# Performance work log

Hardware: AMD Instinct MI355X
Metric: run time of the kernel (lower is better)

The kernel has to match this reference:

```python
import jax, jax.numpy as jnp
import numpy as np

DIM = 1024
B, N = 8, 4096
EPS = 1e-6


def setup_inputs() -> dict:
    key = jax.random.key(0)
    k1, k2, k3, k4 = jax.random.split(key, 4)
    x = jax.random.normal(k1, (B, N, DIM), dtype=jnp.float32)
    # torch nn.Linear weights: W_qkv [3*dim, dim], W_out [dim, dim], b_out [dim]
    s = 1.0 / np.sqrt(DIM)
    W_qkv = jax.random.uniform(k2, (3 * DIM, DIM), jnp.float32, -s, s)
    W_out = jax.random.uniform(k3, (DIM, DIM), jnp.float32, -s, s)
    b_out = jax.random.uniform(k4, (DIM,), jnp.float32, -s, s)
    return {"x": x, "W_qkv": W_qkv, "W_out": W_out, "b_out": b_out}


def reference(x, W_qkv, W_out, b_out):
    # qkv projection (Linear without bias): x @ W_qkv.T -> [B,N,3D]
    qkv = jnp.einsum('bnd,ed->bne', x, W_qkv)
    q, k, v = jnp.split(qkv, 3, axis=-1)
    q = jax.nn.relu(q) + EPS
    k = jax.nn.relu(k) + EPS
    # kv accumulation: [B,D,D]
    kv = jnp.einsum('bnd,bne->bde', k, v)
    # normalizer z: [B,N]
    z = 1.0 / (jnp.einsum('bnd,bd->bn', q, k.sum(axis=1)) + EPS)
    # attn output: [B,N,D]
    attn = jnp.einsum('bnd,bde,bn->bne', q, kv, z)
    # output projection with bias
    return jnp.einsum('bne,fe->bnf', attn, W_out) + b_out
```

## Files before the change

### kernel.cpp

```cpp
#include <hip/hip_runtime.h>


#define EPS 1e-6f

using u16 = unsigned short;
typedef __attribute__((ext_vector_type(4))) float f32x4;
typedef __attribute__((ext_vector_type(8))) __bf16 bf16x8;

__device__ __forceinline__ u16 f2b(float f) {
  unsigned u = __builtin_bit_cast(unsigned, f);
  u += 0x7FFFu + ((u >> 16) & 1u);
  return (u16)(u >> 16);
}
__device__ __forceinline__ float b2f(u16 h) {
  return __builtin_bit_cast(float, (unsigned)h << 16);
}

typedef const __attribute__((address_space(1))) void* gas1_t;
typedef __attribute__((address_space(3))) void* las3_t;

__device__ __forceinline__ void load16_to_lds(const void* g, void* l) {
  __builtin_amdgcn_global_load_lds((gas1_t)g, (las3_t)l, 16, 0, 0);
}

#define BARRIER() do { asm volatile("" ::: "memory"); __builtin_amdgcn_s_barrier(); asm volatile("" ::: "memory"); } while (0)
#define WAITL0()  asm volatile("s_waitcnt lgkmcnt(0)" ::: "memory")
#define WAITV(n)  asm volatile("s_waitcnt vmcnt(" #n ")" ::: "memory")
#define MFMA16(a, b, c) __builtin_amdgcn_mfma_f32_16x16x32_bf16((a), (b), (c), 0, 0, 0)

__device__ __forceinline__ void stage_half(const u16* g, int ld, u16* l,
                                           int r0, int csw, int woff) {
  load16_to_lds(g + (long long)r0 * ld + csw, l + woff);
  load16_to_lds(g + (long long)(r0 + 64) * ld + csw, l + 4096 + woff);
}

template<int MODE>
__global__ __launch_bounds__(512, 2) void gemm256(
    const u16* __restrict__ A, const u16* __restrict__ B, void* __restrict__ Cv,
    int M, int N, int K, int lda, int ldb, int ldc,
    long long sA, long long sB, long long sC,
    const float* __restrict__ zvec, const float* __restrict__ bias,
    u16* __restrict__ kT, u16* __restrict__ vT, float* __restrict__ ksum)
{
  __shared__ __align__(16) u16 shA[32768];
  __shared__ __align__(16) u16 shB[32768];

  const int tid  = threadIdx.x;
  const int lane = tid & 63, wave = tid >> 6;
  const int wr = wave >> 2, wc = wave & 3;
  const int quad = lane >> 4, lc = lane & 15;

  const int TN = gridDim.y;
  const int lin = blockIdx.x + gridDim.x * blockIdx.y;
  const int xcd = lin & 7, g = lin >> 3;
  const int bm = (g / TN) * 8 + xcd;
  const int bn = g % TN;
  const int bz = blockIdx.z;
  const u16* Ab = A + (long long)bz * sA;
  const u16* Bb = B + (long long)bz * sB;

  const int r0   = tid >> 3;
  const int csw  = (((tid & 7) ^ ((tid >> 3) & 7)) << 3);
  const int woff = wave * 512;

  const int ch0 = ((quad ^ (lane & 7)) << 3);
  const int ch1 = (((4 + quad) ^ (lane & 7)) << 3);
  const int aRow = wr * 128 + lc;
  const int bRow = wc * 64 + lc;

  const int NT = K >> 6;

  f32x4 acc[8][4];
  #pragma unroll
  for (int i = 0; i < 8; ++i)
    #pragma unroll
    for (int j = 0; j < 4; ++j) acc[i][j] = f32x4{0.f, 0.f, 0.f, 0.f};

  auto stA = [&](int h, int t) {
    stage_half(Ab + ((long long)bm * 256 + h * 128) * lda + t * 64, lda,
               shA + (t & 1) * 16384 + h * 8192, r0, csw, woff);
  };
  auto stB = [&](int h, int t) {
    stage_half(Bb + ((long long)bn * 256 + h * 128) * ldb + t * 64, ldb,
               shB + (t & 1) * 16384 + h * 8192, r0, csw, woff);
  };

  stA(0, 0); stA(1, 0); stB(0, 0); stB(1, 0);
  if (NT > 1) { stA(0, 1); stA(1, 1); stB(0, 1); WAITV(6); }
  else        { WAITV(0); }
  BARRIER();

  for (int t = 0; t < NT; ++t) {
    const u16* aB = shA + (t & 1) * 16384;
    const u16* bB = shB + (t & 1) * 16384;
    bf16x8 aF[4][2], b01[2][2], b23[2][2];

    #pragma unroll
    for (int i = 0; i < 4; ++i) {
      aF[i][0] = *(const bf16x8*)&aB[(aRow + i * 16) * 64 + ch0];
      aF[i][1] = *(const bf16x8*)&aB[(aRow + i * 16) * 64 + ch1];
    }
    #pragma unroll
    for (int j = 0; j < 2; ++j) {
      b01[j][0] = *(const bf16x8*)&bB[(bRow + j * 16) * 64 + ch0];
      b01[j][1] = *(const bf16x8*)&bB[(bRow + j * 16) * 64 + ch1];
    }
    if (t + 1 < NT) stB(1, t + 1);
    BARRIER(); WAITL0();
    __builtin_amdgcn_s_setprio(1);
    #pragma unroll
    for (int i = 0; i < 4; ++i)
      #pragma unroll
      for (int j = 0; j < 2; ++j) {
        acc[i][j] = MFMA16(aF[i][0], b01[j][0], acc[i][j]);
        acc[i][j] = MFMA16(aF[i][1], b01[j][1], acc[i][j]);
      }
    __builtin_amdgcn_s_setprio(0);
    BARRIER();

    #pragma unroll
    for (int j = 0; j < 2; ++j) {
      b23[j][0] = *(const bf16x8*)&bB[(bRow + (2 + j) * 16) * 64 + ch0];
      b23[j][1] = *(const bf16x8*)&bB[(bRow + (2 + j) * 16) * 64 + ch1];
    }
    BARRIER(); WAITL0();
    __builtin_amdgcn_s_setprio(1);
    #pragma unroll
    for (int i = 0; i < 4; ++i)
      #pragma unroll
      for (int j = 0; j < 2; ++j) {
        acc[i][2 + j] = MFMA16(aF[i][0], b23[j][0], acc[i][2 + j]);
        acc[i][2 + j] = MFMA16(aF[i][1], b23[j][1], acc[i][2 + j]);
      }
    __builtin_amdgcn_s_setprio(0);
    BARRIER();

    #pragma unroll
    for (int i = 0; i < 4; ++i) {
      aF[i][0] = *(const bf16x8*)&aB[(aRow + (4 + i) * 16) * 64 + ch0];
      aF[i][1] = *(const bf16x8*)&aB[(aRow + (4 + i) * 16) * 64 + ch1];
    }
    if (t + 2 < NT) stB(0, t + 2);
    BARRIER(); WAITL0();
    __builtin_amdgcn_s_setprio(1);
    #pragma unroll
    for (int i = 0; i < 4; ++i)
      #pragma unroll
      for (int j = 0; j < 2; ++j) {
        acc[4 + i][j] = MFMA16(aF[i][0], b01[j][0], acc[4 + i][j]);
        acc[4 + i][j] = MFMA16(aF[i][1], b01[j][1], acc[4 + i][j]);
      }
    __builtin_amdgcn_s_setprio(0);
    BARRIER();

    if (t + 2 < NT) { stA(0, t + 2); stA(1, t + 2); }
    BARRIER(); WAITL0();
    __builtin_amdgcn_s_setprio(1);
    #pragma unroll
    for (int i = 0; i < 4; ++i)
      #pragma unroll
      for (int j = 0; j < 2; ++j) {
        acc[4 + i][2 + j] = MFMA16(aF[i][0], b23[j][0], acc[4 + i][2 + j]);
        acc[4 + i][2 + j] = MFMA16(aF[i][1], b23[j][1], acc[4 + i][2 + j]);
      }
    __builtin_amdgcn_s_setprio(0);
    if (t + 2 < NT) { WAITV(6); } else { WAITV(0); }
    BARRIER();
  }

  const long long rowb = (long long)bm * 256 + wr * 128 + quad * 4;
  const int colb = bn * 256 + wc * 64 + lc;

  if (MODE == 0) {
    const int region = colb >> 10;
    if (region == 0) {
      u16* q = (u16*)Cv;
      #pragma unroll
      for (int i = 0; i < 8; ++i)
        #pragma unroll
        for (int j = 0; j < 4; ++j) {
          const int col = colb + j * 16;
          #pragma unroll
          for (int r = 0; r < 4; ++r) {
            const long long row = rowb + i * 16 + r;
            q[row * ldc + col] = f2b(fmaxf(acc[i][j][r], 0.f) + EPS);
          }
        }
    } else {
      const bool isk = (region == 1);
      const int b = (int)(rowb >> 12);
      u16* dst = (isk ? kT : vT) + (long long)b * 1024 * 4096;
      const int nloc = (int)(rowb & 4095);
      #pragma unroll
      for (int j = 0; j < 4; ++j) {
        const int d = colb + j * 16 - region * 1024;
        float s = 0.f;
        #pragma unroll
        for (int i = 0; i < 8; ++i) {
          ushort4 pk;
          #pragma unroll
          for (int r = 0; r < 4; ++r) {
            float v = acc[i][j][r];
            if (isk) { v = fmaxf(v, 0.f) + EPS; s += v; }
            (&pk.x)[r] = f2b(v);
          }
          *(ushort4*)(dst + (long long)d * 4096 + nloc + i * 16) = pk;
        }
        if (isk) {
          s += __shfl_xor(s, 16);
          s += __shfl_xor(s, 32);
          if (quad == 0) atomicAdd(&ksum[b * 1024 + d], s);
        }
      }
    }
  } else if (MODE == 2) {
    float* out = (float*)Cv + (long long)bz * sC;
    #pragma unroll
    for (int i = 0; i < 8; ++i)
      #pragma unroll
      for (int j = 0; j < 4; ++j) {
        const int col = colb + j * 16;
        const float bj = bias[col];
        #pragma unroll
        for (int r = 0; r < 4; ++r) {
          const long long row = rowb + i * 16 + r;
          out[row * ldc + col] = acc[i][j][r] * zvec[(long long)bz * M + row] + bj;
        }
      }
  } else {
    u16* out = (u16*)Cv + (long long)bz * sC;
    #pragma unroll
    for (int i = 0; i < 8; ++i)
      #pragma unroll
      for (int j = 0; j < 4; ++j) {
        const int col = colb + j * 16;
        #pragma unroll
        for (int r = 0; r < 4; ++r) {
          const long long row = rowb + i * 16 + r;
          out[row * ldc + col] = f2b(acc[i][j][r]);
        }
      }
  }
}

template<int MODE>
__global__ __launch_bounds__(256) void gemm_abT(
    const u16* __restrict__ A, const u16* __restrict__ B, void* __restrict__ Cv,
    int M, int N, int K, int lda, int ldb, int ldc,
    long long sA, long long sB, long long sC,
    const float* __restrict__ zvec, const float* __restrict__ bias,
    u16* __restrict__ kT, u16* __restrict__ vT, float* __restrict__ ksum)
{
  __shared__ u16 lA[128 * 32];
  __shared__ u16 lB[128 * 32];
  const int tid  = threadIdx.x;
  const int wave = tid >> 6, lane = tid & 63;
  const int TN = gridDim.y;
  const int lin = blockIdx.x + gridDim.x * blockIdx.y;
  const int xcd = lin & 7, g = lin >> 3;
  const int bm = (g / TN) * 8 + xcd;
  const int bn = g % TN;
  const int bz = blockIdx.z;
  const u16* Ab = A + (long long)bz * sA;
  const u16* Bb = B + (long long)bz * sB;

  const int c0 = wave * 64 + lane;
  const int c1 = 256 + c0;
  const u16* gA0 = Ab + (long long)(bm * 128 + (c0 >> 2)) * lda + (c0 & 3) * 8;
  const u16* gA1 = Ab + (long long)(bm * 128 + (c1 >> 2)) * lda + (c1 & 3) * 8;
  const u16* gB0 = Bb + (long long)(bn * 128 + (c0 >> 2)) * ldb + (c0 & 3) * 8;
  const u16* gB1 = Bb + (long long)(bn * 128 + (c1 >> 2)) * ldb + (c1 & 3) * 8;
  u16* lA0 = &lA[(wave * 64) * 8];
  u16* lA1 = &lA[(256 + wave * 64) * 8];
  u16* lB0 = &lB[(wave * 64) * 8];
  u16* lB1 = &lB[(256 + wave * 64) * 8];

  const int wm = (wave & 1) * 64, wn = (wave >> 1) * 64;
  const int aoff = (wm + (lane & 15)) * 32 + (lane >> 4) * 8;
  const int boff = (wn + (lane & 15)) * 32 + (lane >> 4) * 8;

  f32x4 acc[4][4];
  #pragma unroll
  for (int i = 0; i < 4; i++)
    #pragma unroll
    for (int j = 0; j < 4; j++) acc[i][j] = f32x4{0.f, 0.f, 0.f, 0.f};

  for (int k0 = 0; k0 < K; k0 += 32) {
    load16_to_lds(gA0 + k0, lA0);
    load16_to_lds(gA1 + k0, lA1);
    load16_to_lds(gB0 + k0, lB0);
    load16_to_lds(gB1 + k0, lB1);
    __syncthreads();
    bf16x8 af[4], bfv[4];
    #pragma unroll
    for (int i = 0; i < 4; i++) af[i]  = *(const bf16x8*)&lA[aoff + i * 16 * 32];
    #pragma unroll
    for (int j = 0; j < 4; j++) bfv[j] = *(const bf16x8*)&lB[boff + j * 16 * 32];
    #pragma unroll
    for (int i = 0; i < 4; i++)
      #pragma unroll
      for (int j = 0; j < 4; j++)
        acc[i][j] = MFMA16(af[i], bfv[j], acc[i][j]);
    __syncthreads();
  }

  const int quad = lane >> 4, lc = lane & 15;
  const int rowb = bm * 128 + wm + quad * 4;
  const int colb = bn * 128 + wn + lc;

  #pragma unroll
  for (int i = 0; i < 4; i++) {
    #pragma unroll
    for (int j = 0; j < 4; j++) {
      const int col = colb + j * 16;
      float bj = 0.f;
      if (MODE == 2) bj = bias[col];
      #pragma unroll
      for (int r = 0; r < 4; r++) {
        const int row = rowb + i * 16 + r;
        float v = acc[i][j][r];
        if (MODE == 1) {
          ((u16*)Cv + (long long)bz * sC)[(long long)row * ldc + col] = f2b(v);
        } else if (MODE == 2) {
          float zz = zvec[(long long)bz * M + row];
          ((float*)Cv + (long long)bz * sC)[(long long)row * ldc + col] = v * zz + bj;
        }
      }
    }
  }
  (void)kT; (void)vT; (void)ksum;
}

__global__ void cvt_f32_bf16(const float* __restrict__ s, u16* __restrict__ d, int n4) {
  int i = blockIdx.x * blockDim.x + threadIdx.x;
  int st = gridDim.x * blockDim.x;
  for (; i < n4; i += st) {
    float4 f = ((const float4*)s)[i];
    uint2 o;
    o.x = (unsigned)f2b(f.x) | ((unsigned)f2b(f.y) << 16);
    o.y = (unsigned)f2b(f.z) | ((unsigned)f2b(f.w) << 16);
    ((uint2*)d)[i] = o;
  }
}

__global__ void zero_f32(float* __restrict__ p, int n) {
  int i = blockIdx.x * blockDim.x + threadIdx.x;
  if (i < n) p[i] = 0.f;
}

__global__ void z_kernel(const u16* __restrict__ qbuf, const float* __restrict__ ksum,
                         float* __restrict__ z) {
  const int row  = blockIdx.x * 4 + (threadIdx.x >> 6);
  const int lane = threadIdx.x & 63;
  const int b = row >> 12;
  const uint4* q = (const uint4*)(qbuf + (long long)row * 1024);
  const float* ks = ksum + b * 1024;
  float s = 0.f;
  #pragma unroll
  for (int c = 0; c < 2; c++) {
    int idx = lane + c * 64;
    uint4 d = q[idx];
    unsigned w[4] = {d.x, d.y, d.z, d.w};
    const float* kk = ks + idx * 8;
    #pragma unroll
    for (int qq = 0; qq < 4; qq++)
      s += b2f((u16)(w[qq] & 0xFFFF)) * kk[qq * 2]
         + b2f((u16)(w[qq] >> 16))    * kk[qq * 2 + 1];
  }
  #pragma unroll
  for (int o = 32; o > 0; o >>= 1) s += __shfl_down(s, o);
  if (lane == 0) z[row] = 1.0f / (s + EPS);
}

extern "C" void kernel_launch(void* const* d_in, const int* in_sizes, int n_in,
                              void* d_out, int out_size, void* d_ws, size_t ws_size,
                              hipStream_t stream) {
  const float* x    = (const float*)d_in[0];
  const float* Wqkv = (const float*)d_in[1];
  const float* Wout = (const float*)d_in[2];
  const float* bout = (const float*)d_in[3];

  char* ws = (char*)d_ws;
  u16* x_bf    = (u16*)(ws + 0);
  u16* qbuf    = (u16*)(ws + 67108864);
  u16* kT      = (u16*)(ws + 134217728);
  u16* vT      = (u16*)(ws + 201326592);
  u16* wqkv_bf = (u16*)(ws + 268435456);
  u16* wout_bf = (u16*)(ws + 274726912);
  u16* kv      = (u16*)(ws + 276824064);
  u16* kvwT    = (u16*)(ws + 293601280);
  float* ksum  = (float*)(ws + 310378496);
  float* z     = (float*)(ws + 310411264);

  cvt_f32_bf16<<<4096, 256, 0, stream>>>(x,    x_bf,    33554432 / 4);
  cvt_f32_bf16<<<1024, 256, 0, stream>>>(Wqkv, wqkv_bf,  3145728 / 4);
  cvt_f32_bf16<<<512,  256, 0, stream>>>(Wout, wout_bf,  1048576 / 4);
  zero_f32<<<32, 256, 0, stream>>>(ksum, 8192);

  gemm256<0><<<dim3(128, 12, 1), 512, 0, stream>>>(
      x_bf, wqkv_bf, qbuf, 32768, 3072, 1024, 1024, 1024, 1024,
      0, 0, 0, nullptr, nullptr, kT, vT, ksum);

  z_kernel<<<8192, 256, 0, stream>>>(qbuf, ksum, z);

  gemm_abT<1><<<dim3(8, 8, 8), 256, 0, stream>>>(
      kT, vT, kv, 1024, 1024, 4096, 4096, 4096, 1024,
      4194304, 4194304, 1048576, nullptr, nullptr, nullptr, nullptr, nullptr);

  gemm_abT<1><<<dim3(8, 8, 8), 256, 0, stream>>>(
      wout_bf, kv, kvwT, 1024, 1024, 1024, 1024, 1024, 1024,
      0, 1048576, 1048576, nullptr, nullptr, nullptr, nullptr, nullptr);

  gemm256<2><<<dim3(16, 4, 8), 512, 0, stream>>>(
      qbuf, kvwT, d_out, 4096, 1024, 1024, 1024, 1024, 1024,
      4194304, 1048576, 4194304, z, bout, nullptr, nullptr, nullptr);
}
```

Baseline: 708.6 us.

## Prefetch next tile's A fragments during last MFMA phase of GEMM loop

Moves the LDS read of the first half of A fragments for the next K-tile into the final phase of the current iteration, using a separate register set for the second half so the two can overlap. The global-load wait moves earlier so the next buffer is ready before that prefetch, and a sched_barrier is added after LDS waits to pin the instruction order. The aim is to hide LDS latency at the start of each iteration, at the cost of extra registers that may pressure occupancy at 2 waves per SIMD.

```diff
diff --git a/kernel.cpp b/kernel.cpp
--- a/kernel.cpp
+++ b/kernel.cpp
@@ -24,7 +24,7 @@
 }
 
 #define BARRIER() do { asm volatile("" ::: "memory"); __builtin_amdgcn_s_barrier(); asm volatile("" ::: "memory"); } while (0)
-#define WAITL0()  asm volatile("s_waitcnt lgkmcnt(0)" ::: "memory")
+#define WAITL0()  do { asm volatile("s_waitcnt lgkmcnt(0)" ::: "memory"); __builtin_amdgcn_sched_barrier(0); } while (0)
 #define WAITV(n)  asm volatile("s_waitcnt vmcnt(" #n ")" ::: "memory")
 #define MFMA16(a, b, c) __builtin_amdgcn_mfma_f32_16x16x32_bf16((a), (b), (c), 0, 0, 0)
 
@@ -85,21 +85,23 @@
                shB + (t & 1) * 16384 + h * 8192, r0, csw, woff);
   };
 
+  bf16x8 aF[4][2], aG[4][2], b01[2][2], b23[2][2];
+
   stA(0, 0); stA(1, 0); stB(0, 0); stB(1, 0);
-  if (NT > 1) { stA(0, 1); stA(1, 1); stB(0, 1); WAITV(6); }
+  if (NT > 1) { stB(0, 1); stA(0, 1); stA(1, 1); WAITV(6); }
   else        { WAITV(0); }
   BARRIER();
+  #pragma unroll
+  for (int i = 0; i < 4; ++i) {
+    aF[i][0] = *(const bf16x8*)&shA[(aRow + i * 16) * 64 + ch0];
+    aF[i][1] = *(const bf16x8*)&shA[(aRow + i * 16) * 64 + ch1];
+  }
 
   for (int t = 0; t < NT; ++t) {
     const u16* aB = shA + (t & 1) * 16384;
     const u16* bB = shB + (t & 1) * 16384;
-    bf16x8 aF[4][2], b01[2][2], b23[2][2];
-
-    #pragma unroll
-    for (int i = 0; i < 4; ++i) {
-      aF[i][0] = *(const bf16x8*)&aB[(aRow + i * 16) * 64 + ch0];
-      aF[i][1] = *(const bf16x8*)&aB[(aRow + i * 16) * 64 + ch1];
-    }
+    const u16* aN = shA + ((t + 1) & 1) * 16384;
+
     #pragma unroll
     for (int j = 0; j < 2; ++j) {
       b01[j][0] = *(const bf16x8*)&bB[(bRow + j * 16) * 64 + ch0];
@@ -137,8 +139,8 @@
 
     #pragma unroll
     for (int i = 0; i < 4; ++i) {
-      aF[i][0] = *(const bf16x8*)&aB[(aRow + (4 + i) * 16) * 64 + ch0];
-      aF[i][1] = *(const bf16x8*)&aB[(aRow + (4 + i) * 16) * 64 + ch1];
+      aG[i][0] = *(const bf16x8*)&aB[(aRow + (4 + i) * 16) * 64 + ch0];
+      aG[i][1] = *(const bf16x8*)&aB[(aRow + (4 + i) * 16) * 64 + ch1];
     }
     if (t + 2 < NT) stB(0, t + 2);
     BARRIER(); WAITL0();
@@ -147,24 +149,31 @@
     for (int i = 0; i < 4; ++i)
       #pragma unroll
       for (int j = 0; j < 2; ++j) {
-        acc[4 + i][j] = MFMA16(aF[i][0], b01[j][0], acc[4 + i][j]);
-        acc[4 + i][j] = MFMA16(aF[i][1], b01[j][1], acc[4 + i][j]);
+        acc[4 + i][j] = MFMA16(aG[i][0], b01[j][0], acc[4 + i][j]);
+        acc[4 + i][j] = MFMA16(aG[i][1], b01[j][1], acc[4 + i][j]);
       }
     __builtin_amdgcn_s_setprio(0);
+    if (t + 2 < NT) { WAITV(2); } else { WAITV(0); }
     BARRIER();
 
+    if (t + 1 < NT) {
+      #pragma unroll
+      for (int i = 0; i < 4; ++i) {
+        aF[i][0] = *(const bf16x8*)&aN[(aRow + i * 16) * 64 + ch0];
+        aF[i][1] = *(const bf16x8*)&aN[(aRow + i * 16) * 64 + ch1];
+      }
+    }
     if (t + 2 < NT) { stA(0, t + 2); stA(1, t + 2); }
-    BARRIER(); WAITL0();
+    BARRIER();
     __builtin_amdgcn_s_setprio(1);
     #pragma unroll
     for (int i = 0; i < 4; ++i)
       #pragma unroll
       for (int j = 0; j < 2; ++j) {
-        acc[4 + i][2 + j] = MFMA16(aF[i][0], b23[j][0], acc[4 + i][2 + j]);
-        acc[4 + i][2 + j] = MFMA16(aF[i][1], b23[j][1], acc[4 + i][2 + j]);
+        acc[4 + i][2 + j] = MFMA16(aG[i][0], b23[j][0], acc[4 + i][2 + j]);
+        acc[4 + i][2 + j] = MFMA16(aG[i][1], b23[j][1], acc[4 + i][2 + j]);
       }
     __builtin_amdgcn_s_setprio(0);
-    if (t + 2 < NT) { WAITV(6); } else { WAITV(0); }
     BARRIER();
   }
 
```

Result: no change. 711.5 us (+0.4%).

## Split-K the per-batch KV GEMM with 256-tile kernel and separate reduction

Applied to the files above, without the earlier changes.

Replaces the gemm_abT KV accumulation (K=4096) with the larger 256-tile gemm256 kernel in a new mode that splits K into two halves across 16 z-slices. Each half writes fp32 partials into the now-unused x_bf workspace. A new reduce_kv kernel sums the halves and converts them to bf16. The aim is better per-block efficiency and enough blocks to fill the device, at the cost of an extra kernel launch and a round trip of fp32 partials through memory. Grid remapping also skips the XCD swizzle when gridDim.x < 8.

```diff
diff --git a/kernel.cpp b/kernel.cpp
--- a/kernel.cpp
+++ b/kernel.cpp
@@ -52,12 +52,26 @@
 
   const int TN = gridDim.y;
   const int lin = blockIdx.x + gridDim.x * blockIdx.y;
-  const int xcd = lin & 7, g = lin >> 3;
-  const int bm = (g / TN) * 8 + xcd;
-  const int bn = g % TN;
+  int bm, bn;
+  if (gridDim.x >= 8) {
+    const int xcd = lin & 7, g = lin >> 3;
+    bm = (g / TN) * 8 + xcd;
+    bn = g % TN;
+  } else {
+    bm = blockIdx.x;
+    bn = blockIdx.y;
+  }
   const int bz = blockIdx.z;
-  const u16* Ab = A + (long long)bz * sA;
-  const u16* Bb = B + (long long)bz * sB;
+  const u16* Ab;
+  const u16* Bb;
+  if (MODE == 3) {
+    const int bb = bz & 7, kh = bz >> 3;
+    Ab = A + (long long)bb * sA + kh * 2048;
+    Bb = B + (long long)bb * sB + kh * 2048;
+  } else {
+    Ab = A + (long long)bz * sA;
+    Bb = B + (long long)bz * sB;
+  }
 
   const int r0   = tid >> 3;
   const int csw  = (((tid & 7) ^ ((tid >> 3) & 7)) << 3);
@@ -225,6 +239,19 @@
         for (int r = 0; r < 4; ++r) {
           const long long row = rowb + i * 16 + r;
           out[row * ldc + col] = acc[i][j][r] * zvec[(long long)bz * M + row] + bj;
+        }
+      }
+  } else if (MODE == 3) {
+    float* out = (float*)Cv + (long long)bz * sC;
+    #pragma unroll
+    for (int i = 0; i < 8; ++i)
+      #pragma unroll
+      for (int j = 0; j < 4; ++j) {
+        const int col = colb + j * 16;
+        #pragma unroll
+        for (int r = 0; r < 4; ++r) {
+          const long long row = rowb + i * 16 + r;
+          out[row * ldc + col] = acc[i][j][r];
         }
       }
   } else {
@@ -348,6 +375,23 @@
   if (i < n) p[i] = 0.f;
 }
 
+__global__ void reduce_kv(const float* __restrict__ p, u16* __restrict__ kv) {
+  long long idx = blockIdx.x * blockDim.x + threadIdx.x;
+  const long long st = (long long)gridDim.x * blockDim.x;
+  for (; idx < 2097152; idx += st) {
+    const long long b = idx >> 18;
+    const long long i = idx & 262143;
+    float4 x = ((const float4*)p)[b * 262144 + i];
+    float4 y = ((const float4*)p)[(8 + b) * 262144 + i];
+    float4 s;
+    s.x = x.x + y.x; s.y = x.y + y.y; s.z = x.z + y.z; s.w = x.w + y.w;
+    uint2 o;
+    o.x = (unsigned)f2b(s.x) | ((unsigned)f2b(s.y) << 16);
+    o.y = (unsigned)f2b(s.z) | ((unsigned)f2b(s.w) << 16);
+    ((uint2*)kv)[b * 262144 + i] = o;
+  }
+}
+
 __global__ void z_kernel(const u16* __restrict__ qbuf, const float* __restrict__ ksum,
                          float* __restrict__ z) {
   const int row  = blockIdx.x * 4 + (threadIdx.x >> 6);
@@ -403,9 +447,11 @@
 
   z_kernel<<<8192, 256, 0, stream>>>(qbuf, ksum, z);
 
-  gemm_abT<1><<<dim3(8, 8, 8), 256, 0, stream>>>(
-      kT, vT, kv, 1024, 1024, 4096, 4096, 4096, 1024,
+  gemm256<3><<<dim3(4, 4, 16), 512, 0, stream>>>(
+      kT, vT, (float*)x_bf, 1024, 1024, 2048, 4096, 4096, 1024,
       4194304, 4194304, 1048576, nullptr, nullptr, nullptr, nullptr, nullptr);
+
+  reduce_kv<<<2048, 256, 0, stream>>>((const float*)x_bf, kv);
 
   gemm_abT<1><<<dim3(8, 8, 8), 256, 0, stream>>>(
       wout_bf, kv, kvwT, 1024, 1024, 1024, 1024, 1024, 1024,
```

Result: no change. 697.4 us (-1.6%).
